# Performance work log

Measured on AMD Instinct MI355X. Metric: run time of the kernel, lower is better.

Reference implementation:

```python
import jax, jax.numpy as jnp
import numpy as np

B, S, I, H, O = 4096, 512, 28, 128, 28

def setup_inputs() -> dict:
    key = jax.random.key(0)
    ks = jax.random.split(key, 7)
    s = lambda fan_in: 1.0 / np.sqrt(fan_in)
    return {
        "x":    jax.random.normal(ks[0], (B, S, I), dtype=jnp.float32),
        "W_ih": jax.random.uniform(ks[1], (I, H), jnp.float32, -s(I), s(I)),
        "b_ih": jax.random.uniform(ks[2], (H,),  jnp.float32, -s(I), s(I)),
        "W_hh": jax.random.uniform(ks[3], (H, H), jnp.float32, -s(H), s(H)),
        "b_hh": jax.random.uniform(ks[4], (H,),  jnp.float32, -s(H), s(H)),
        "W_ho": jax.random.uniform(ks[5], (H, O), jnp.float32, -s(H), s(H)),
        "b_ho": jax.random.uniform(ks[6], (O,),  jnp.float32, -s(H), s(H)),
    }

def reference(x, W_ih, b_ih, W_hh, b_hh, W_ho, b_ho):
    # Precompute input projections for all timesteps in one big GEMM: [B,S,H]
    xproj = jnp.einsum("bsi,ih->bsh", x, W_ih) + b_ih
    h0 = jnp.zeros((x.shape[0], W_hh.shape[0]), dtype=x.dtype)

    def step(h, xp_t):
        h = jnp.tanh(xp_t + h @ W_hh + b_hh)
        return h, None

    # scan over time axis: xproj transposed to [S,B,H]
    h_final, _ = jax.lax.scan(step, h0, jnp.swapaxes(xproj, 0, 1))
    return h_final @ W_ho + b_ho
```

## Files before the change

kernel.cpp:

```cpp
#include <hip/hip_runtime.h>
#include <stdint.h>

#define S_LEN 512
#define I_DIM 28
#define H_DIM 128
#define O_DIM 28
#define BT    16

typedef __attribute__((ext_vector_type(8))) short bf16x8;
typedef __attribute__((ext_vector_type(4))) float f32x4;

static __device__ __forceinline__ short f2bf(float f) {
    unsigned u = __float_as_uint(f);
    u = (u + 0x7fffu + ((u >> 16) & 1u)) >> 16;
    return (short)u;
}
static __device__ __forceinline__ float bf2f(unsigned short u) {
    return __uint_as_float(((unsigned)u) << 16);
}
static __device__ __forceinline__ unsigned cvt_pk(float a, float b) {
    unsigned r;
    asm("v_cvt_pk_bf16_f32 %0, %1, %2" : "=v"(r) : "v"(a), "v"(b));
    return r;
}
#define TWO_LOG2E 2.8853900817779268f
static __device__ __forceinline__ float fast_tanh(float a) {
    float e = __builtin_amdgcn_exp2f(a * TWO_LOG2E);
    float r = __builtin_amdgcn_rcpf(1.0f + e);
    return fmaf(-2.0f, r, 1.0f);
}

__global__ __launch_bounds__(256, 1) void rnn_fused(
    const float* __restrict__ x,
    const float* __restrict__ W_ih, const float* __restrict__ b_ih,
    const float* __restrict__ W_hh, const float* __restrict__ b_hh,
    const float* __restrict__ W_ho, const float* __restrict__ b_ho,
    float* __restrict__ out)
{
    const int tid  = threadIdx.x;
    const int wave = tid >> 6;
    const int lane = tid & 63;
    const int l15  = lane & 15;
    const int lk   = lane >> 4;
    const int r0   = blockIdx.x * BT;

    __shared__ __align__(16) bf16x8 hx[2][4][64];
    __shared__ __align__(16) bf16x8 xring[8][64];

    bf16x8 Arel[2][4];
    bf16x8 Aih[2];
    f32x4  biasv[2];
    const int jmA = 32 * wave + ((l15 >> 2) << 3) + (l15 & 3);
    #pragma unroll
    for (int T = 0; T < 2; ++T) {
        const int jA = jmA + 4 * T;
        #pragma unroll
        for (int q = 0; q < 4; ++q) {
            const int kc = (wave + q) & 3;
            #pragma unroll
            for (int e = 0; e < 8; ++e)
                Arel[T][q][e] = f2bf(W_hh[(kc * 32 + lk * 8 + e) * H_DIM + jA]);
        }
        #pragma unroll
        for (int e = 0; e < 8; ++e) {
            int i = lk * 8 + e;
            Aih[T][e] = (i < I_DIM) ? f2bf(W_ih[i * H_DIM + jA]) : (short)0;
        }
        #pragma unroll
        for (int r = 0; r < 4; ++r) {
            int jC = 32 * wave + lk * 8 + 4 * T + r;
            biasv[T][r] = b_ih[jC] + b_hh[jC];
        }
    }

    const int o1 = ((wave + 1) & 3) * 64 + lane;
    const int o2 = ((wave + 2) & 3) * 64 + lane;
    const int o3 = ((wave + 3) & 3) * 64 + lane;

    bf16x8 bown = {0,0,0,0,0,0,0,0};
    hx[0][wave][lane] = bown;

    const bool hasHi = (lk < 3);
    const float* xbase = x + (size_t)(r0 + l15) * S_LEN * I_DIM + lk * 8;

    {
        const float* src = xbase + wave * I_DIM;
        float4 lo = *(const float4*)src;
        float4 hi = hasHi ? *(const float4*)(src + 4) : make_float4(0.f,0.f,0.f,0.f);
        union { bf16x8 v; unsigned u[4]; } fr;
        fr.u[0] = cvt_pk(lo.x, lo.y); fr.u[1] = cvt_pk(lo.z, lo.w);
        fr.u[2] = cvt_pk(hi.x, hi.y); fr.u[3] = cvt_pk(hi.z, hi.w);
        xring[wave][lane] = fr.v;
    }
    asm volatile("s_waitcnt lgkmcnt(0)" ::: "memory");
    __builtin_amdgcn_s_barrier();
    asm volatile("" ::: "memory");

    bf16x8 xcur = xring[0][lane];

#define RSTEP(PAR, P)                                                          \
    {                                                                          \
        const bf16x8* hxp = &hx[PAR][0][0];                                    \
        bf16x8 g1 = hxp[o1];                                                   \
        bf16x8 g2 = hxp[o2];                                                   \
        bf16x8 g3 = hxp[o3];                                                   \
        bf16x8 xnext = xring[(t4 + P + 1) & 7][lane];                          \
        if (P == 0 && tf < S_LEN) {                                            \
            const float* src = xbase + (size_t)tf * I_DIM;                     \
            pf_lo = *(const float4*)src;                                       \
            if (hasHi) pf_hi = *(const float4*)(src + 4);                      \
        }                                                                      \
        f32x4 a0 = biasv[0], a1 = biasv[1];                                    \
        a0 = __builtin_amdgcn_mfma_f32_16x16x32_bf16(Aih[0],     xcur, a0, 0,0,0); \
        a1 = __builtin_amdgcn_mfma_f32_16x16x32_bf16(Aih[1],     xcur, a1, 0,0,0); \
        a0 = __builtin_amdgcn_mfma_f32_16x16x32_bf16(Arel[0][0], bown, a0, 0,0,0); \
        a1 = __builtin_amdgcn_mfma_f32_16x16x32_bf16(Arel[1][0], bown, a1, 0,0,0); \
        f32x4 c0 = {0.f,0.f,0.f,0.f}, c1 = {0.f,0.f,0.f,0.f};                  \
        c0 = __builtin_amdgcn_mfma_f32_16x16x32_bf16(Arel[0][1], g1, c0, 0,0,0); \
        c1 = __builtin_amdgcn_mfma_f32_16x16x32_bf16(Arel[1][1], g1, c1, 0,0,0); \
        a0 = __builtin_amdgcn_mfma_f32_16x16x32_bf16(Arel[0][2], g2, a0, 0,0,0); \
        a1 = __builtin_amdgcn_mfma_f32_16x16x32_bf16(Arel[1][2], g2, a1, 0,0,0); \
        c0 = __builtin_amdgcn_mfma_f32_16x16x32_bf16(Arel[0][3], g3, c0, 0,0,0); \
        c1 = __builtin_amdgcn_mfma_f32_16x16x32_bf16(Arel[1][3], g3, c1, 0,0,0); \
        if (P == 2 && tf < S_LEN) {                                            \
            union { bf16x8 v; unsigned u[4]; } fr;                             \
            fr.u[0] = cvt_pk(pf_lo.x, pf_lo.y); fr.u[1] = cvt_pk(pf_lo.z, pf_lo.w); \
            fr.u[2] = cvt_pk(pf_hi.x, pf_hi.y); fr.u[3] = cvt_pk(pf_hi.z, pf_hi.w); \
            xring[tf & 7][lane] = fr.v;                                        \
        }                                                                      \
        f32x4 s0 = a0 + c0, s1 = a1 + c1;                                      \
        float h0_ = fast_tanh(s0[0]), h1_ = fast_tanh(s0[1]);                  \
        float h2_ = fast_tanh(s0[2]), h3_ = fast_tanh(s0[3]);                  \
        float h4_ = fast_tanh(s1[0]), h5_ = fast_tanh(s1[1]);                  \
        float h6_ = fast_tanh(s1[2]), h7_ = fast_tanh(s1[3]);                  \
        union { bf16x8 v; unsigned u[4]; } hf;                                 \
        hf.u[0] = cvt_pk(h0_, h1_); hf.u[1] = cvt_pk(h2_, h3_);                \
        hf.u[2] = cvt_pk(h4_, h5_); hf.u[3] = cvt_pk(h6_, h7_);                \
        hx[(PAR) ^ 1][wave][lane] = hf.v;                                      \
        bown = hf.v;                                                           \
        asm volatile("s_waitcnt lgkmcnt(0)" ::: "memory");                     \
        __builtin_amdgcn_s_barrier();                                          \
        asm volatile("" ::: "memory");                                        \
        xcur = xnext;                                                          \
    }

    for (int t4 = 0; t4 < S_LEN; t4 += 4) {
        const int tf = t4 + 4 + wave;
        float4 pf_lo = make_float4(0.f,0.f,0.f,0.f), pf_hi = pf_lo;
        RSTEP(0, 0)
        RSTEP(1, 1)
        RSTEP(0, 2)
        RSTEP(1, 3)
    }
#undef RSTEP

    for (int idx = tid; idx < BT * O_DIM; idx += 256) {
        const int b = idx / O_DIM;
        const int o = idx - b * O_DIM;
        float sum = b_ho[o];
        const unsigned short* hb = (const unsigned short*)&hx[0][0][0];
        #pragma unroll 4
        for (int j = 0; j < H_DIM; ++j) {
            int slot = (j >> 5) * 64 + ((j >> 3) & 3) * 16 + b;
            sum += bf2f(hb[slot * 8 + (j & 7)]) * W_ho[j * O_DIM + o];
        }
        out[(size_t)(r0 + b) * O_DIM + o] = sum;
    }
}

extern "C" void kernel_launch(void* const* d_in, const int* in_sizes, int n_in,
                              void* d_out, int out_size, void* d_ws, size_t ws_size,
                              hipStream_t stream) {
    const float* x    = (const float*)d_in[0];
    const float* W_ih = (const float*)d_in[1];
    const float* b_ih = (const float*)d_in[2];
    const float* W_hh = (const float*)d_in[3];
    const float* b_hh = (const float*)d_in[4];
    const float* W_ho = (const float*)d_in[5];
    const float* b_ho = (const float*)d_in[6];
    const int B = in_sizes[0] / (S_LEN * I_DIM);
    rnn_fused<<<B / BT, 256, 0, stream>>>(x, W_ih, b_ih, W_hh, b_hh, W_ho, b_ho,
                                          (float*)d_out);
}
```

Measured before the change: 187.2 us.

## Split recurrence across 8 waves per block and use Pade tanh

Doubles the block to 512 threads so each of 8 waves computes 16 hidden units per step instead of 32. This halves the per-wave MFMA chain and the tanh work on the serial critical path. The hidden-state exchange layout is rebuilt so all four chunks are read from LDS, and the x ring is widened to 16 steps. The exp-based tanh is replaced by a clamped Pade rational approximation. The costs are a barrier across more waves each step, and possible accuracy differences from the Pade tanh at large inputs.

Result: faster. 183.2 us (-2.1%).

```diff
diff --git a/kernel.cpp b/kernel.cpp
--- a/kernel.cpp
+++ b/kernel.cpp
@@ -23,14 +23,15 @@
     asm("v_cvt_pk_bf16_f32 %0, %1, %2" : "=v"(r) : "v"(a), "v"(b));
     return r;
 }
-#define TWO_LOG2E 2.8853900817779268f
-static __device__ __forceinline__ float fast_tanh(float a) {
-    float e = __builtin_amdgcn_exp2f(a * TWO_LOG2E);
-    float r = __builtin_amdgcn_rcpf(1.0f + e);
-    return fmaf(-2.0f, r, 1.0f);
+static __device__ __forceinline__ float pade_tanh(float x) {
+    float u = x * x;
+    float n = fmaf(u, fmaf(u, 1.0f, 105.0f), 945.0f) * x;
+    float d = fmaf(u, fmaf(u, 15.0f, 420.0f), 945.0f);
+    float t = n * __builtin_amdgcn_rcpf(d);
+    return fminf(fmaxf(t, -1.0f), 1.0f);
 }
 
-__global__ __launch_bounds__(256, 1) void rnn_fused(
+__global__ __launch_bounds__(512, 1) void rnn_fused(
     const float* __restrict__ x,
     const float* __restrict__ W_ih, const float* __restrict__ b_ih,
     const float* __restrict__ W_hh, const float* __restrict__ b_hh,
@@ -45,40 +46,31 @@
     const int r0   = blockIdx.x * BT;
 
     __shared__ __align__(16) bf16x8 hx[2][4][64];
-    __shared__ __align__(16) bf16x8 xring[8][64];
+    __shared__ __align__(16) bf16x8 xring[16][64];
 
-    bf16x8 Arel[2][4];
-    bf16x8 Aih[2];
-    f32x4  biasv[2];
-    const int jmA = 32 * wave + ((l15 >> 2) << 3) + (l15 & 3);
+    bf16x8 Ahh0, Ahh1, Ahh2, Ahh3, Aih;
+    f32x4  biasv;
+    const int jA = 16 * wave + l15;
     #pragma unroll
-    for (int T = 0; T < 2; ++T) {
-        const int jA = jmA + 4 * T;
-        #pragma unroll
-        for (int q = 0; q < 4; ++q) {
-            const int kc = (wave + q) & 3;
-            #pragma unroll
-            for (int e = 0; e < 8; ++e)
-                Arel[T][q][e] = f2bf(W_hh[(kc * 32 + lk * 8 + e) * H_DIM + jA]);
-        }
-        #pragma unroll
-        for (int e = 0; e < 8; ++e) {
-            int i = lk * 8 + e;
-            Aih[T][e] = (i < I_DIM) ? f2bf(W_ih[i * H_DIM + jA]) : (short)0;
-        }
-        #pragma unroll
-        for (int r = 0; r < 4; ++r) {
-            int jC = 32 * wave + lk * 8 + 4 * T + r;
-            biasv[T][r] = b_ih[jC] + b_hh[jC];
-        }
+    for (int e = 0; e < 8; ++e) {
+        Ahh0[e] = f2bf(W_hh[(  0 + lk * 8 + e) * H_DIM + jA]);
+        Ahh1[e] = f2bf(W_hh[( 32 + lk * 8 + e) * H_DIM + jA]);
+        Ahh2[e] = f2bf(W_hh[( 64 + lk * 8 + e) * H_DIM + jA]);
+        Ahh3[e] = f2bf(W_hh[( 96 + lk * 8 + e) * H_DIM + jA]);
+        int i = lk * 8 + e;
+        Aih[e] = (i < I_DIM) ? f2bf(W_ih[i * H_DIM + jA]) : (short)0;
+    }
+    #pragma unroll
+    for (int r = 0; r < 4; ++r) {
+        int jC = 16 * wave + lk * 4 + r;
+        biasv[r] = b_ih[jC] + b_hh[jC];
     }
 
-    const int o1 = ((wave + 1) & 3) * 64 + lane;
-    const int o2 = ((wave + 2) & 3) * 64 + lane;
-    const int o3 = ((wave + 3) & 3) * 64 + lane;
+    const int wboff = (wave >> 1) * 1024
+                    + ((2 * (wave & 1) + (lk >> 1)) * 16 + l15) * 16
+                    + 8 * (lk & 1);
 
-    bf16x8 bown = {0,0,0,0,0,0,0,0};
-    hx[0][wave][lane] = bown;
+    ((uint2*)&hx[0][0][0])[tid] = make_uint2(0u, 0u);
 
     const bool hasHi = (lk < 3);
     const float* xbase = x + (size_t)(r0 + l15) * S_LEN * I_DIM + lk * 8;
@@ -96,65 +88,59 @@
     __builtin_amdgcn_s_barrier();
     asm volatile("" ::: "memory");
 
-    bf16x8 xcur = xring[0][lane];
-
 #define RSTEP(PAR, P)                                                          \
     {                                                                          \
         const bf16x8* hxp = &hx[PAR][0][0];                                    \
-        bf16x8 g1 = hxp[o1];                                                   \
-        bf16x8 g2 = hxp[o2];                                                   \
-        bf16x8 g3 = hxp[o3];                                                   \
-        bf16x8 xnext = xring[(t4 + P + 1) & 7][lane];                          \
-        if (P == 0 && tf < S_LEN) {                                            \
+        bf16x8 b0 = hxp[0 * 64 + lane];                                        \
+        bf16x8 b1 = hxp[1 * 64 + lane];                                        \
+        bf16x8 b2 = hxp[2 * 64 + lane];                                        \
+        bf16x8 b3 = hxp[3 * 64 + lane];                                        \
+        bf16x8 xc = xring[(t8 + P) & 15][lane];                                \
+        if (P == 0 && doPf) {                                                  \
             const float* src = xbase + (size_t)tf * I_DIM;                     \
             pf_lo = *(const float4*)src;                                       \
             if (hasHi) pf_hi = *(const float4*)(src + 4);                      \
         }                                                                      \
-        f32x4 a0 = biasv[0], a1 = biasv[1];                                    \
-        a0 = __builtin_amdgcn_mfma_f32_16x16x32_bf16(Aih[0],     xcur, a0, 0,0,0); \
-        a1 = __builtin_amdgcn_mfma_f32_16x16x32_bf16(Aih[1],     xcur, a1, 0,0,0); \
-        a0 = __builtin_amdgcn_mfma_f32_16x16x32_bf16(Arel[0][0], bown, a0, 0,0,0); \
-        a1 = __builtin_amdgcn_mfma_f32_16x16x32_bf16(Arel[1][0], bown, a1, 0,0,0); \
-        f32x4 c0 = {0.f,0.f,0.f,0.f}, c1 = {0.f,0.f,0.f,0.f};                  \
-        c0 = __builtin_amdgcn_mfma_f32_16x16x32_bf16(Arel[0][1], g1, c0, 0,0,0); \
-        c1 = __builtin_amdgcn_mfma_f32_16x16x32_bf16(Arel[1][1], g1, c1, 0,0,0); \
-        a0 = __builtin_amdgcn_mfma_f32_16x16x32_bf16(Arel[0][2], g2, a0, 0,0,0); \
-        a1 = __builtin_amdgcn_mfma_f32_16x16x32_bf16(Arel[1][2], g2, a1, 0,0,0); \
-        c0 = __builtin_amdgcn_mfma_f32_16x16x32_bf16(Arel[0][3], g3, c0, 0,0,0); \
-        c1 = __builtin_amdgcn_mfma_f32_16x16x32_bf16(Arel[1][3], g3, c1, 0,0,0); \
-        if (P == 2 && tf < S_LEN) {                                            \
+        f32x4 a = biasv;                                                       \
+        a = __builtin_amdgcn_mfma_f32_16x16x32_bf16(Aih,  xc, a, 0, 0, 0);     \
+        a = __builtin_amdgcn_mfma_f32_16x16x32_bf16(Ahh0, b0, a, 0, 0, 0);     \
+        a = __builtin_amdgcn_mfma_f32_16x16x32_bf16(Ahh1, b1, a, 0, 0, 0);     \
+        f32x4 c = {0.f, 0.f, 0.f, 0.f};                                        \
+        c = __builtin_amdgcn_mfma_f32_16x16x32_bf16(Ahh2, b2, c, 0, 0, 0);     \
+        c = __builtin_amdgcn_mfma_f32_16x16x32_bf16(Ahh3, b3, c, 0, 0, 0);     \
+        if (P == 2 && doPf) {                                                  \
             union { bf16x8 v; unsigned u[4]; } fr;                             \
             fr.u[0] = cvt_pk(pf_lo.x, pf_lo.y); fr.u[1] = cvt_pk(pf_lo.z, pf_lo.w); \
             fr.u[2] = cvt_pk(pf_hi.x, pf_hi.y); fr.u[3] = cvt_pk(pf_hi.z, pf_hi.w); \
-            xring[tf & 7][lane] = fr.v;                                        \
+            xring[tf & 15][lane] = fr.v;                                       \
         }                                                                      \
-        f32x4 s0 = a0 + c0, s1 = a1 + c1;                                      \
-        float h0_ = fast_tanh(s0[0]), h1_ = fast_tanh(s0[1]);                  \
-        float h2_ = fast_tanh(s0[2]), h3_ = fast_tanh(s0[3]);                  \
-        float h4_ = fast_tanh(s1[0]), h5_ = fast_tanh(s1[1]);                  \
-        float h6_ = fast_tanh(s1[2]), h7_ = fast_tanh(s1[3]);                  \
-        union { bf16x8 v; unsigned u[4]; } hf;                                 \
-        hf.u[0] = cvt_pk(h0_, h1_); hf.u[1] = cvt_pk(h2_, h3_);                \
-        hf.u[2] = cvt_pk(h4_, h5_); hf.u[3] = cvt_pk(h6_, h7_);                \
-        hx[(PAR) ^ 1][wave][lane] = hf.v;                                      \
-        bown = hf.v;                                                           \
+        f32x4 s = a + c;                                                       \
+        float h0_ = pade_tanh(s[0]), h1_ = pade_tanh(s[1]);                    \
+        float h2_ = pade_tanh(s[2]), h3_ = pade_tanh(s[3]);                    \
+        uint2 wv;                                                              \
+        wv.x = cvt_pk(h0_, h1_); wv.y = cvt_pk(h2_, h3_);                      \
+        *(uint2*)((char*)&hx[(PAR) ^ 1][0][0] + wboff) = wv;                   \
         asm volatile("s_waitcnt lgkmcnt(0)" ::: "memory");                     \
         __builtin_amdgcn_s_barrier();                                          \
         asm volatile("" ::: "memory");                                        \
-        xcur = xnext;                                                          \
     }
 
-    for (int t4 = 0; t4 < S_LEN; t4 += 4) {
-        const int tf = t4 + 4 + wave;
+    for (int t8 = 0; t8 < S_LEN; t8 += 8) {
+        const int tf   = t8 + 8 + wave;
+        const bool doPf = (tf < S_LEN);
         float4 pf_lo = make_float4(0.f,0.f,0.f,0.f), pf_hi = pf_lo;
         RSTEP(0, 0)
         RSTEP(1, 1)
         RSTEP(0, 2)
         RSTEP(1, 3)
+        RSTEP(0, 4)
+        RSTEP(1, 5)
+        RSTEP(0, 6)
+        RSTEP(1, 7)
     }
 #undef RSTEP
 
-    for (int idx = tid; idx < BT * O_DIM; idx += 256) {
+    for (int idx = tid; idx < BT * O_DIM; idx += 512) {
         const int b = idx / O_DIM;
         const int o = idx - b * O_DIM;
         float sum = b_ho[o];
@@ -179,6 +165,6 @@
     const float* W_ho = (const float*)d_in[5];
     const float* b_ho = (const float*)d_in[6];
     const int B = in_sizes[0] / (S_LEN * I_DIM);
-    rnn_fused<<<B / BT, 256, 0, stream>>>(x, W_ih, b_ih, W_hh, b_hh, W_ho, b_ho,
+    rnn_fused<<<B / BT, 512, 0, stream>>>(x, W_ih, b_ih, W_hh, b_hh, W_ho, b_ho,
                                           (float*)d_out);
 }
```
